# Kernel optimization log

Measured on AMD Instinct MI355X. Metric: run time of the kernel, lower is better.

The kernel has to match this reference:

```python
import jax, jax.numpy as jnp
import numpy as np

DIM = 4096
N_HEADS = 32
N_KV_HEADS = 8
HEAD_DIM = 128
ROPE_THETA = 10000.0
REPEATS = N_HEADS // N_KV_HEADS
SCALE = HEAD_DIM ** -0.5


def rope(x, seq_len, offset):
    # x: [b, h, seq_len, head_dim]; faithful to source: cos/sin from cat((freqs,freqs)),
    # rotate built by interleaved pair swap then flatten.
    d = x.shape[-1]
    inv_freq = 1.0 / (ROPE_THETA ** (jnp.arange(0, d, 2, dtype=jnp.float32) / d))  # [d/2]
    t = jnp.arange(offset, offset + seq_len, dtype=jnp.float32)                    # [L]
    freqs = t[:, None] * inv_freq[None, :]                                         # [L, d/2]
    emb = jnp.concatenate([freqs, freqs], axis=-1)                                 # [L, d]
    cos_emb = jnp.cos(emb)
    sin_emb = jnp.sin(emb)
    x_even = x[..., 0::2]
    x_odd = x[..., 1::2]
    rotate_x = jnp.stack([-x_odd, x_even], axis=-1).reshape(x.shape)
    return x * cos_emb + rotate_x * sin_emb


def setup_inputs() -> dict:
    key = jax.random.key(0)
    k1, k2, k3, k4, k5 = jax.random.split(key, 5)
    b, l = 1, 2048
    s = 0.02
    x = jax.random.normal(k1, (b, l, DIM), dtype=jnp.float32)
    wq = jax.random.normal(k2, (DIM, N_HEADS * HEAD_DIM), dtype=jnp.float32) * s
    wk = jax.random.normal(k3, (DIM, N_KV_HEADS * HEAD_DIM), dtype=jnp.float32) * s
    wv = jax.random.normal(k4, (DIM, N_KV_HEADS * HEAD_DIM), dtype=jnp.float32) * s
    wo = jax.random.normal(k5, (N_HEADS * HEAD_DIM, DIM), dtype=jnp.float32) * s
    return {"x": x, "wq": wq, "wk": wk, "wv": wv, "wo": wo, "seq_len": l}


def reference(x, wq, wk, wv, wo, seq_len):
    b, l, _ = x.shape
    q = (x @ wq).reshape(b, l, N_HEADS, HEAD_DIM).transpose(0, 2, 1, 3)       # [b,H,l,d]
    k = (x @ wk).reshape(b, l, N_KV_HEADS, HEAD_DIM).transpose(0, 2, 1, 3)    # [b,Hk,l,d]
    v = (x @ wv).reshape(b, l, N_KV_HEADS, HEAD_DIM).transpose(0, 2, 1, 3)
    # repeat KV heads to match query heads (GQA)
    k = jnp.repeat(k, REPEATS, axis=1)   # [b,H,l,d]
    v = jnp.repeat(v, REPEATS, axis=1)
    offset = 0  # cache is None
    q = rope(q, seq_len, offset)
    k = rope(k, seq_len, offset)
    scores = jnp.einsum('bhid,bhjd->bhij', q * SCALE, k)
    scores = jax.nn.softmax(scores.astype(jnp.float32), axis=-1).astype(scores.dtype)
    out = jnp.einsum('bhij,bhjd->bhid', scores, v)
    out = out.transpose(0, 2, 1, 3).reshape(b, l, N_HEADS * HEAD_DIM)
    return out @ wo, (k, v)
```

## Files before the change

kernel.cpp:

```cpp
#include <hip/hip_runtime.h>
#include <cstdint>
#include <cstddef>

#define DIM 4096
#define SEQ 2048
#define NH 32
#define NKV 8
#define HD 128
#define QKVN 6144

typedef __bf16 bf16_t;
typedef __bf16 bf16x8 __attribute__((ext_vector_type(8)));
typedef __bf16 bf16x4 __attribute__((ext_vector_type(4)));
typedef __bf16 bf16x2 __attribute__((ext_vector_type(2)));
typedef float f32x4 __attribute__((ext_vector_type(4)));
typedef int int4v __attribute__((ext_vector_type(4)));

__device__ __forceinline__ f32x4 mfma16(bf16x8 a, bf16x8 b, f32x4 c) {
  return __builtin_amdgcn_mfma_f32_16x16x32_bf16(a, b, c, 0, 0, 0);
}

__device__ __forceinline__ void async16(const bf16_t* g, bf16_t* l) {
  __builtin_amdgcn_global_load_lds((__attribute__((address_space(1))) void*)g,
                                   (__attribute__((address_space(3))) void*)l,
                                   16, 0, 0);
}

__device__ __forceinline__ int pack2(float a, float b) {
  bf16x2 h = { (bf16_t)a, (bf16_t)b };
  return __builtin_bit_cast(int, h);
}

#define LGKM0() do { asm volatile("s_waitcnt lgkmcnt(0)" ::: "memory"); \
                     __builtin_amdgcn_sched_barrier(0); } while (0)
#define VM0() do { asm volatile("s_waitcnt vmcnt(0)" ::: "memory"); } while (0)

__global__ void cast_x(const float* __restrict__ x, bf16_t* __restrict__ xb) {
  int i = blockIdx.x * 256 + threadIdx.x;
  const float4 v = ((const float4*)x)[i];
  bf16x4 o = { (bf16_t)v.x, (bf16_t)v.y, (bf16_t)v.z, (bf16_t)v.w };
  *(bf16x4*)(xb + (size_t)i * 4) = o;
}

__global__ void tcast(const float* __restrict__ src, bf16_t* __restrict__ dst,
                      int Ncols, int Kdim) {
  __shared__ float tile[32][33];
  int n0 = blockIdx.x * 32, k0 = blockIdx.y * 32;
  int tx = threadIdx.x, ty = threadIdx.y;
#pragma unroll
  for (int r = 0; r < 4; r++)
    tile[ty + 8 * r][tx] = src[(size_t)(k0 + ty + 8 * r) * Ncols + n0 + tx];
  __syncthreads();
#pragma unroll
  for (int r = 0; r < 4; r++)
    dst[(size_t)(n0 + ty + 8 * r) * Kdim + k0 + tx] = (bf16_t)tile[tx][ty + 8 * r];
}

__global__ __launch_bounds__(512) void gemm256(const bf16_t* __restrict__ A,
                                               const bf16_t* __restrict__ Bt,
                                               float* __restrict__ C,
                                               int M, int N, int K) {
  __shared__ bf16_t As[2][16384];
  __shared__ bf16_t Bs[2][16384];
  const int t = threadIdx.x;
  const int lane = t & 63;
  const int l15 = lane & 15, quad = lane >> 4;
  const int w = t >> 6, wm = w >> 2, wn = w & 3;

  const int gx = gridDim.x;
  const int nwg = gx * gridDim.y;
  const int id = blockIdx.y * gx + blockIdx.x;
  const int swz = (id & 7) * (nwg >> 3) + (id >> 3);
  const int bm = (swz / gx) * 256, bn = (swz % gx) * 256;

  const int srow = t >> 3;
  const int scol = ((t & 7) << 3) ^ ((t >> 1) & 16);
  const bf16_t* gA = A + (size_t)(bm + srow) * K + scol;
  const bf16_t* gB = Bt + (size_t)(bn + srow) * K + scol;
  const int ldst = t * 8;

  const int qx = (quad * 8) ^ ((l15 & 4) ? 16 : 0);
  const int aBase = wm * 8192 + l15 * 64 + qx;
  const int bBase = (wn >> 1) * 8192 + ((wn & 1) * 64 + l15) * 64 + qx;

  f32x4 acc[8][4] = {};
  bf16x8 af[4][2], bfr[2][2];

#pragma unroll
  for (int h = 0; h < 2; h++)
#pragma unroll
    for (int i = 0; i < 2; i++) {
      async16(gA + (size_t)(h * 128 + i * 64) * K, &As[0][h * 8192 + i * 4096 + ldst]);
      async16(gB + (size_t)(h * 128 + i * 64) * K, &Bs[0][h * 8192 + i * 4096 + ldst]);
    }
  VM0();
  __builtin_amdgcn_s_barrier();

  const int nkt = K >> 6;
  for (int kt = 0; kt < nkt; ++kt) {
    const int buf = kt & 1;
    const int k1 = (kt + 1) << 6;
    const bool pf = (kt + 1) < nkt;

#pragma unroll
    for (int mi = 0; mi < 4; mi++)
#pragma unroll
      for (int s = 0; s < 2; s++)
        af[mi][s] = *(const bf16x8*)&As[buf][aBase + mi * 1024 + s * 32];
#pragma unroll
    for (int ni = 0; ni < 2; ni++)
#pragma unroll
      for (int s = 0; s < 2; s++)
        bfr[ni][s] = *(const bf16x8*)&Bs[buf][bBase + ni * 1024 + s * 32];
    if (pf) {
#pragma unroll
      for (int h = 0; h < 2; h++)
#pragma unroll
        for (int i = 0; i < 2; i++)
          async16(gA + (size_t)(h * 128 + i * 64) * K + k1,
                  &As[buf ^ 1][h * 8192 + i * 4096 + ldst]);
    }
    __builtin_amdgcn_s_barrier();
    LGKM0();
    __builtin_amdgcn_s_setprio(1);
#pragma unroll
    for (int mi = 0; mi < 4; mi++)
#pragma unroll
      for (int ni = 0; ni < 2; ni++)
#pragma unroll
        for (int s = 0; s < 2; s++)
          acc[mi][ni] = mfma16(af[mi][s], bfr[ni][s], acc[mi][ni]);
    __builtin_amdgcn_s_setprio(0);
    __builtin_amdgcn_s_barrier();

#pragma unroll
    for (int ni = 0; ni < 2; ni++)
#pragma unroll
      for (int s = 0; s < 2; s++)
        bfr[ni][s] = *(const bf16x8*)&Bs[buf][bBase + (ni + 2) * 1024 + s * 32];
    if (pf) {
#pragma unroll
      for (int h = 0; h < 2; h++)
#pragma unroll
        for (int i = 0; i < 2; i++)
          async16(gB + (size_t)(h * 128 + i * 64) * K + k1,
                  &Bs[buf ^ 1][h * 8192 + i * 4096 + ldst]);
    }
    __builtin_amdgcn_s_barrier();
    LGKM0();
    __builtin_amdgcn_s_setprio(1);
#pragma unroll
    for (int mi = 0; mi < 4; mi++)
#pragma unroll
      for (int ni = 0; ni < 2; ni++)
#pragma unroll
        for (int s = 0; s < 2; s++)
          acc[mi][ni + 2] = mfma16(af[mi][s], bfr[ni][s], acc[mi][ni + 2]);
    __builtin_amdgcn_s_setprio(0);
    __builtin_amdgcn_s_barrier();

#pragma unroll
    for (int mi = 0; mi < 4; mi++)
#pragma unroll
      for (int s = 0; s < 2; s++)
        af[mi][s] = *(const bf16x8*)&As[buf][aBase + (mi + 4) * 1024 + s * 32];
    __builtin_amdgcn_s_barrier();
    LGKM0();
    __builtin_amdgcn_s_setprio(1);
#pragma unroll
    for (int mi = 0; mi < 4; mi++)
#pragma unroll
      for (int ni = 0; ni < 2; ni++)
#pragma unroll
        for (int s = 0; s < 2; s++)
          acc[mi + 4][ni + 2] = mfma16(af[mi][s], bfr[ni][s], acc[mi + 4][ni + 2]);
    __builtin_amdgcn_s_setprio(0);
    __builtin_amdgcn_s_barrier();

#pragma unroll
    for (int ni = 0; ni < 2; ni++)
#pragma unroll
      for (int s = 0; s < 2; s++)
        bfr[ni][s] = *(const bf16x8*)&Bs[buf][bBase + ni * 1024 + s * 32];
    __builtin_amdgcn_s_barrier();
    LGKM0();
    __builtin_amdgcn_s_setprio(1);
#pragma unroll
    for (int mi = 0; mi < 4; mi++)
#pragma unroll
      for (int ni = 0; ni < 2; ni++)
#pragma unroll
        for (int s = 0; s < 2; s++)
          acc[mi + 4][ni] = mfma16(af[mi][s], bfr[ni][s], acc[mi + 4][ni]);
    __builtin_amdgcn_s_setprio(0);
    VM0();
    __builtin_amdgcn_s_barrier();
  }

#pragma unroll
  for (int mi = 0; mi < 8; mi++)
#pragma unroll
    for (int ni = 0; ni < 4; ni++) {
      size_t row = (size_t)bm + wm * 128 + mi * 16 + quad * 4;
      size_t col = (size_t)bn + wn * 64 + ni * 16 + l15;
#pragma unroll
      for (int r = 0; r < 4; r++)
        C[(row + r) * N + col] = acc[mi][ni][r];
    }
}

__global__ void rope_scatter(const float* __restrict__ qkv, bf16_t* __restrict__ Qb,
                             bf16_t* __restrict__ Kb, bf16_t* __restrict__ Vt,
                             float* __restrict__ kOut, float* __restrict__ vOut) {
  int idx = blockIdx.x * 256 + threadIdx.x;
  int t = idx / 3072;
  int p = idx - t * 3072;
  const float NEG_L2T_64 = -0.20762050593046f;
  const float SS = 0.08838834764831845f * 1.4426950408889634f;
  if (p < 2048) {
    int hh = p >> 6, pr = p & 63;
    int d0 = pr << 1;
    const float* src = qkv + (size_t)t * QKVN + hh * HD + d0;
    float a = src[0], b = src[1];
    int j0 = d0 & 63, j1 = (d0 + 1) & 63;
    float th0 = (float)t * exp2f((float)j0 * NEG_L2T_64);
    float th1 = (float)t * exp2f((float)j1 * NEG_L2T_64);
    float o0 = (a * cosf(th0) - b * sinf(th0)) * SS;
    float o1 = (b * cosf(th1) + a * sinf(th1)) * SS;
    bf16_t* dst = Qb + ((size_t)hh * SEQ + t) * HD + d0;
    dst[0] = (bf16_t)o0;
    dst[1] = (bf16_t)o1;
  } else if (p < 2560) {
    int q2 = p - 2048;
    int kh = q2 >> 6, pr = q2 & 63;
    int d0 = pr << 1;
    const float* src = qkv + (size_t)t * QKVN + 4096 + kh * HD + d0;
    float a = src[0], b = src[1];
    int j0 = d0 & 63, j1 = (d0 + 1) & 63;
    float th0 = (float)t * exp2f((float)j0 * NEG_L2T_64);
    float th1 = (float)t * exp2f((float)j1 * NEG_L2T_64);
    float o0 = a * cosf(th0) - b * sinf(th0);
    float o1 = b * cosf(th1) + a * sinf(th1);
    bf16_t* dst = Kb + ((size_t)kh * SEQ + t) * HD + d0;
    dst[0] = (bf16_t)o0;
    dst[1] = (bf16_t)o1;
#pragma unroll
    for (int rep = 0; rep < 4; rep++) {
      float* kp = kOut + ((size_t)(kh * 4 + rep) * SEQ + t) * HD + d0;
      kp[0] = o0;
      kp[1] = o1;
    }
  } else {
    int q2 = p - 2560;
    int kh = q2 >> 6, pr = q2 & 63;
    int d0 = pr << 1;
    const float* src = qkv + (size_t)t * QKVN + 5120 + kh * HD + d0;
    float a = src[0], b = src[1];
#pragma unroll
    for (int rep = 0; rep < 4; rep++) {
      float* vp = vOut + ((size_t)(kh * 4 + rep) * SEQ + t) * HD + d0;
      vp[0] = a;
      vp[1] = b;
    }
    int tp = (t & ~31) + ((t & 12) << 1) + (t & 3) + ((t & 16) >> 2);
    Vt[((size_t)kh * HD + d0) * SEQ + tp] = (bf16_t)a;
    Vt[((size_t)kh * HD + d0 + 1) * SEQ + tp] = (bf16_t)b;
  }
}

__global__ __launch_bounds__(512, 2) void attn_kernel(const bf16_t* __restrict__ Qb,
                                                      const bf16_t* __restrict__ Kb,
                                                      const bf16_t* __restrict__ Vt,
                                                      bf16_t* __restrict__ AO) {
  __shared__ bf16_t Ks[2][8192];
  __shared__ bf16_t Vs[2][8192];
  const int h = blockIdx.y, kh = h >> 2;
  const int qbase = blockIdx.x * 256;
  const int w = threadIdx.x >> 6, lane = threadIdx.x & 63;
  const int l15 = lane & 15, quad = lane >> 4;
  const bf16_t* KbH = Kb + (size_t)kh * SEQ * HD;
  const bf16_t* VtH = Vt + (size_t)kh * HD * SEQ;

  bf16x8 qf[2][4];
#pragma unroll
  for (int nq = 0; nq < 2; nq++) {
    const bf16_t* qp = Qb + ((size_t)h * SEQ + qbase + w * 32 + nq * 16 + l15) * HD + quad * 8;
#pragma unroll
    for (int kc = 0; kc < 4; kc++) qf[nq][kc] = *(const bf16x8*)(qp + kc * 32);
  }

  f32x4 acc[8][2] = {};
  float rsum[2] = {0.f, 0.f};

  auto stage = [&](int buf, int kt0) {
    if (w < 4) {
      int kc = w;
#pragma unroll
      for (int kg = 0; kg < 4; kg++) {
        const bf16_t* g = KbH + (size_t)(kt0 + kg * 16 + (lane >> 2)) * HD + kc * 32 + (lane & 3) * 8;
        async16(g, &Ks[buf][kc * 2048 + kg * 512]);
      }
    } else {
      int vi = w - 4, kt = vi >> 1, dg0 = (vi & 1) * 4;
#pragma unroll
      for (int j = 0; j < 4; j++) {
        int dg = dg0 + j;
        const bf16_t* g = VtH + (size_t)(dg * 16 + (lane >> 2)) * SEQ + kt0 + kt * 32 + (lane & 3) * 8;
        async16(g, &Vs[buf][kt * 4096 + dg * 512]);
      }
    }
  };

  stage(0, 0);
  int buf = 0;

  for (int kt0 = 0; kt0 < SEQ; kt0 += 64, buf ^= 1) {
    __syncthreads();
    if (kt0 + 64 < SEQ) stage(buf ^ 1, kt0 + 64);

    f32x4 sacc[4][2] = {};
#pragma unroll
    for (int mi = 0; mi < 4; mi++)
#pragma unroll
      for (int kc = 0; kc < 4; kc++) {
        bf16x8 kf = *(const bf16x8*)(&Ks[buf][(kc * 64 + mi * 16 + l15) * 32 + quad * 8]);
#pragma unroll
        for (int nq = 0; nq < 2; nq++)
          sacc[mi][nq] = mfma16(kf, qf[nq][kc], sacc[mi][nq]);
      }

    int pk[4][2][2];
#pragma unroll
    for (int mi = 0; mi < 4; mi++)
#pragma unroll
      for (int nq = 0; nq < 2; nq++) {
        float p0 = exp2f(sacc[mi][nq][0]);
        float p1 = exp2f(sacc[mi][nq][1]);
        float p2 = exp2f(sacc[mi][nq][2]);
        float p3 = exp2f(sacc[mi][nq][3]);
        rsum[nq] += (p0 + p1) + (p2 + p3);
        pk[mi][nq][0] = pack2(p0, p1);
        pk[mi][nq][1] = pack2(p2, p3);
      }

#pragma unroll
    for (int kt = 0; kt < 2; kt++) {
#pragma unroll
      for (int nq = 0; nq < 2; nq++) {
        int4v dw;
        dw[0] = pk[2 * kt][nq][0];
        dw[1] = pk[2 * kt][nq][1];
        dw[2] = pk[2 * kt + 1][nq][0];
        dw[3] = pk[2 * kt + 1][nq][1];
        bf16x8 pf = __builtin_bit_cast(bf16x8, dw);
#pragma unroll
        for (int dt = 0; dt < 8; dt++) {
          bf16x8 vf = *(const bf16x8*)(&Vs[buf][(kt * 128 + dt * 16 + l15) * 32 + quad * 8]);
          acc[dt][nq] = mfma16(vf, pf, acc[dt][nq]);
        }
      }
    }
  }

#pragma unroll
  for (int nq = 0; nq < 2; nq++) {
    float rs = rsum[nq];
    rs += __shfl_xor(rs, 16);
    rs += __shfl_xor(rs, 32);
    float inv = 1.0f / rs;
    int q = qbase + w * 32 + nq * 16 + l15;
#pragma unroll
    for (int dt = 0; dt < 8; dt++) {
      bf16x4 o = { (bf16_t)(acc[dt][nq][0] * inv), (bf16_t)(acc[dt][nq][1] * inv),
                   (bf16_t)(acc[dt][nq][2] * inv), (bf16_t)(acc[dt][nq][3] * inv) };
      *(bf16x4*)(AO + (size_t)q * DIM + h * HD + dt * 16 + quad * 4) = o;
    }
  }
}

extern "C" void kernel_launch(void* const* d_in, const int* in_sizes, int n_in,
                              void* d_out, int out_size, void* d_ws, size_t ws_size,
                              hipStream_t stream) {
  const float* x = (const float*)d_in[0];
  const float* wq = (const float*)d_in[1];
  const float* wk = (const float*)d_in[2];
  const float* wv = (const float*)d_in[3];
  const float* wo = (const float*)d_in[4];
  float* out = (float*)d_out;
  float* kOut = out + (size_t)SEQ * DIM;
  float* vOut = kOut + (size_t)NH * SEQ * HD;

  char* ws = (char*)d_ws;
  bf16_t* Xb = (bf16_t*)ws;
  bf16_t* WT = (bf16_t*)(ws + 16777216);
  float* QKV = (float*)(ws + 67108864);
  bf16_t* WoT = (bf16_t*)(ws + 67108864);
  bf16_t* Qb = (bf16_t*)(ws + 117440512);
  bf16_t* Kb = (bf16_t*)(ws + 134217728);
  bf16_t* Vt = (bf16_t*)(ws + 138412032);
  bf16_t* AO = Xb;

  dim3 tb(32, 8);
  cast_x<<<8192, 256, 0, stream>>>(x, Xb);
  tcast<<<dim3(128, 128), tb, 0, stream>>>(wq, WT, 4096, 4096);
  tcast<<<dim3(32, 128), tb, 0, stream>>>(wk, WT + (size_t)4096 * 4096, 1024, 4096);
  tcast<<<dim3(32, 128), tb, 0, stream>>>(wv, WT + (size_t)5120 * 4096, 1024, 4096);
  gemm256<<<dim3(24, 8), 512, 0, stream>>>(Xb, WT, QKV, 2048, 6144, 4096);
  rope_scatter<<<24576, 256, 0, stream>>>(QKV, Qb, Kb, Vt, kOut, vOut);
  tcast<<<dim3(128, 128), tb, 0, stream>>>(wo, WoT, 4096, 4096);
  attn_kernel<<<dim3(8, 32), 512, 0, stream>>>(Qb, Kb, Vt, AO);
  gemm256<<<dim3(16, 8), 512, 0, stream>>>(AO, WoT, out, 2048, 4096, 4096);
}
```

Before: 607.5 us.

## Shrink GEMM N-tile to 192/128 columns and stage loads with partial vmcnt waits

The bf16 GEMM is templated on the N-tile width, so the QKV projection uses 256x192 tiles and the output projection uses 256x128 tiles. Both grids grow to 256 workgroups, which fills more compute units than the earlier 192 and 128 tiles. The LDS swizzle becomes a row-based XOR, and the per-stage prefetches are split into three groups with partial vmcnt waits in place of a full drain. The cost is more total global traffic from the narrower tiles, and the hand-counted waits are fragile.

```diff
diff --git a/kernel.cpp b/kernel.cpp
--- a/kernel.cpp
+++ b/kernel.cpp
@@ -33,7 +33,14 @@
 
 #define LGKM0() do { asm volatile("s_waitcnt lgkmcnt(0)" ::: "memory"); \
                      __builtin_amdgcn_sched_barrier(0); } while (0)
-#define VM0() do { asm volatile("s_waitcnt vmcnt(0)" ::: "memory"); } while (0)
+
+template <int N> __device__ __forceinline__ void vmw() {
+  if constexpr (N == 3) asm volatile("s_waitcnt vmcnt(3)" ::: "memory");
+  else if constexpr (N == 4) asm volatile("s_waitcnt vmcnt(4)" ::: "memory");
+  else if constexpr (N == 5) asm volatile("s_waitcnt vmcnt(5)" ::: "memory");
+  else if constexpr (N == 6) asm volatile("s_waitcnt vmcnt(6)" ::: "memory");
+  __builtin_amdgcn_sched_barrier(0);
+}
 
 __global__ void cast_x(const float* __restrict__ x, bf16_t* __restrict__ xb) {
   int i = blockIdx.x * 256 + threadIdx.x;
@@ -56,44 +63,54 @@
     dst[(size_t)(n0 + ty + 8 * r) * Kdim + k0 + tx] = (bf16_t)tile[tx][ty + 8 * r];
 }
 
+template <int NF>
 __global__ __launch_bounds__(512) void gemm256(const bf16_t* __restrict__ A,
                                                const bf16_t* __restrict__ Bt,
                                                float* __restrict__ C,
                                                int M, int N, int K) {
+  constexpr int NA = NF - 1;
+  constexpr int S1 = 2 + NA;
   __shared__ bf16_t As[2][16384];
-  __shared__ bf16_t Bs[2][16384];
+  __shared__ bf16_t Bs[2][NF * 4096];
   const int t = threadIdx.x;
   const int lane = t & 63;
   const int l15 = lane & 15, quad = lane >> 4;
   const int w = t >> 6, wm = w >> 2, wn = w & 3;
+  const int cgx = l15 & 7;
 
   const int gx = gridDim.x;
   const int nwg = gx * gridDim.y;
   const int id = blockIdx.y * gx + blockIdx.x;
   const int swz = (id & 7) * (nwg >> 3) + (id >> 3);
-  const int bm = (swz / gx) * 256, bn = (swz % gx) * 256;
+  const int bm = (swz / gx) * 256, bn = (swz % gx) * (NF * 64);
 
   const int srow = t >> 3;
-  const int scol = ((t & 7) << 3) ^ ((t >> 1) & 16);
+  const int scol = ((t & 7) ^ (srow & 7)) << 3;
   const bf16_t* gA = A + (size_t)(bm + srow) * K + scol;
   const bf16_t* gB = Bt + (size_t)(bn + srow) * K + scol;
   const int ldst = t * 8;
 
-  const int qx = (quad * 8) ^ ((l15 & 4) ? 16 : 0);
-  const int aBase = wm * 8192 + l15 * 64 + qx;
-  const int bBase = (wn >> 1) * 8192 + ((wn & 1) * 64 + l15) * 64 + qx;
-
-  f32x4 acc[8][4] = {};
-  bf16x8 af[4][2], bfr[2][2];
-
-#pragma unroll
-  for (int h = 0; h < 2; h++)
-#pragma unroll
-    for (int i = 0; i < 2; i++) {
-      async16(gA + (size_t)(h * 128 + i * 64) * K, &As[0][h * 8192 + i * 4096 + ldst]);
-      async16(gB + (size_t)(h * 128 + i * 64) * K, &Bs[0][h * 8192 + i * 4096 + ldst]);
-    }
-  VM0();
+  f32x4 acc[8][NF] = {};
+  bf16x8 af[4][2], bfa[NA][2], bfb[2];
+
+  auto sb1 = [&](int b2, int kk) {
+    async16(gA + kk, &As[b2][ldst]);
+    async16(gA + (size_t)64 * K + kk, &As[b2][4096 + ldst]);
+    async16(gB + kk, &Bs[b2][ldst]);
+    if constexpr (NF == 3) async16(gB + (size_t)64 * K + kk, &Bs[b2][4096 + ldst]);
+  };
+  auto sb2 = [&](int b2, int kk) {
+    async16(gB + (size_t)((NF - 1) * 64) * K + kk, &Bs[b2][(NF - 1) * 4096 + ldst]);
+  };
+  auto sb3 = [&](int b2, int kk) {
+    async16(gA + (size_t)128 * K + kk, &As[b2][8192 + ldst]);
+    async16(gA + (size_t)192 * K + kk, &As[b2][12288 + ldst]);
+  };
+
+  sb1(0, 0);
+  sb2(0, 0);
+  sb3(0, 0);
+  vmw<3>();
   __builtin_amdgcn_s_barrier();
 
   const int nkt = K >> 6;
@@ -106,103 +123,91 @@
     for (int mi = 0; mi < 4; mi++)
 #pragma unroll
       for (int s = 0; s < 2; s++)
-        af[mi][s] = *(const bf16x8*)&As[buf][aBase + mi * 1024 + s * 32];
-#pragma unroll
-    for (int ni = 0; ni < 2; ni++)
-#pragma unroll
-      for (int s = 0; s < 2; s++)
-        bfr[ni][s] = *(const bf16x8*)&Bs[buf][bBase + ni * 1024 + s * 32];
-    if (pf) {
-#pragma unroll
-      for (int h = 0; h < 2; h++)
-#pragma unroll
-        for (int i = 0; i < 2; i++)
-          async16(gA + (size_t)(h * 128 + i * 64) * K + k1,
-                  &As[buf ^ 1][h * 8192 + i * 4096 + ldst]);
-    }
+        af[mi][s] = *(const bf16x8*)&As[buf][(wm * 64 + mi * 16 + l15) * 64 +
+                                            (((s << 2) | quad) ^ cgx) * 8];
+#pragma unroll
+    for (int ni = 0; ni < NA; ni++)
+#pragma unroll
+      for (int s = 0; s < 2; s++)
+        bfa[ni][s] = *(const bf16x8*)&Bs[buf][(ni * 64 + wn * 16 + l15) * 64 +
+                                              (((s << 2) | quad) ^ cgx) * 8];
+    if (pf) sb1(buf ^ 1, k1);
     __builtin_amdgcn_s_barrier();
     LGKM0();
     __builtin_amdgcn_s_setprio(1);
 #pragma unroll
     for (int mi = 0; mi < 4; mi++)
 #pragma unroll
-      for (int ni = 0; ni < 2; ni++)
+      for (int ni = 0; ni < NA; ni++)
 #pragma unroll
         for (int s = 0; s < 2; s++)
-          acc[mi][ni] = mfma16(af[mi][s], bfr[ni][s], acc[mi][ni]);
+          acc[mi][ni] = mfma16(af[mi][s], bfa[ni][s], acc[mi][ni]);
     __builtin_amdgcn_s_setprio(0);
-    __builtin_amdgcn_s_barrier();
-
-#pragma unroll
-    for (int ni = 0; ni < 2; ni++)
-#pragma unroll
-      for (int s = 0; s < 2; s++)
-        bfr[ni][s] = *(const bf16x8*)&Bs[buf][bBase + (ni + 2) * 1024 + s * 32];
-    if (pf) {
-#pragma unroll
-      for (int h = 0; h < 2; h++)
-#pragma unroll
-        for (int i = 0; i < 2; i++)
-          async16(gB + (size_t)(h * 128 + i * 64) * K + k1,
-                  &Bs[buf ^ 1][h * 8192 + i * 4096 + ldst]);
-    }
+    vmw<2 + S1>();
+    __builtin_amdgcn_s_barrier();
+
+#pragma unroll
+    for (int s = 0; s < 2; s++)
+      bfb[s] = *(const bf16x8*)&Bs[buf][((NF - 1) * 64 + wn * 16 + l15) * 64 +
+                                        (((s << 2) | quad) ^ cgx) * 8];
+    if (pf) sb2(buf ^ 1, k1);
     __builtin_amdgcn_s_barrier();
     LGKM0();
     __builtin_amdgcn_s_setprio(1);
 #pragma unroll
     for (int mi = 0; mi < 4; mi++)
 #pragma unroll
-      for (int ni = 0; ni < 2; ni++)
-#pragma unroll
-        for (int s = 0; s < 2; s++)
-          acc[mi][ni + 2] = mfma16(af[mi][s], bfr[ni][s], acc[mi][ni + 2]);
+      for (int s = 0; s < 2; s++)
+        acc[mi][NF - 1] = mfma16(af[mi][s], bfb[s], acc[mi][NF - 1]);
     __builtin_amdgcn_s_setprio(0);
-    __builtin_amdgcn_s_barrier();
-
-#pragma unroll
-    for (int mi = 0; mi < 4; mi++)
-#pragma unroll
-      for (int s = 0; s < 2; s++)
-        af[mi][s] = *(const bf16x8*)&As[buf][aBase + (mi + 4) * 1024 + s * 32];
+    vmw<1 + S1>();
+    __builtin_amdgcn_s_barrier();
+
+#pragma unroll
+    for (int mi = 0; mi < 4; mi++)
+#pragma unroll
+      for (int s = 0; s < 2; s++)
+        af[mi][s] = *(const bf16x8*)&As[buf][(128 + wm * 64 + mi * 16 + l15) * 64 +
+                                             (((s << 2) | quad) ^ cgx) * 8];
+    if (pf) sb3(buf ^ 1, k1);
     __builtin_amdgcn_s_barrier();
     LGKM0();
     __builtin_amdgcn_s_setprio(1);
 #pragma unroll
     for (int mi = 0; mi < 4; mi++)
 #pragma unroll
-      for (int ni = 0; ni < 2; ni++)
-#pragma unroll
-        for (int s = 0; s < 2; s++)
-          acc[mi + 4][ni + 2] = mfma16(af[mi][s], bfr[ni][s], acc[mi + 4][ni + 2]);
+      for (int s = 0; s < 2; s++)
+        acc[mi + 4][NF - 1] = mfma16(af[mi][s], bfb[s], acc[mi + 4][NF - 1]);
     __builtin_amdgcn_s_setprio(0);
     __builtin_amdgcn_s_barrier();
 
 #pragma unroll
-    for (int ni = 0; ni < 2; ni++)
-#pragma unroll
-      for (int s = 0; s < 2; s++)
-        bfr[ni][s] = *(const bf16x8*)&Bs[buf][bBase + ni * 1024 + s * 32];
+    for (int ni = 0; ni < NA; ni++)
+#pragma unroll
+      for (int s = 0; s < 2; s++)
+        bfa[ni][s] = *(const bf16x8*)&Bs[buf][(ni * 64 + wn * 16 + l15) * 64 +
+                                              (((s << 2) | quad) ^ cgx) * 8];
     __builtin_amdgcn_s_barrier();
     LGKM0();
     __builtin_amdgcn_s_setprio(1);
 #pragma unroll
     for (int mi = 0; mi < 4; mi++)
 #pragma unroll
-      for (int ni = 0; ni < 2; ni++)
+      for (int ni = 0; ni < NA; ni++)
 #pragma unroll
         for (int s = 0; s < 2; s++)
-          acc[mi + 4][ni] = mfma16(af[mi][s], bfr[ni][s], acc[mi + 4][ni]);
+          acc[mi + 4][ni] = mfma16(af[mi][s], bfa[ni][s], acc[mi + 4][ni]);
     __builtin_amdgcn_s_setprio(0);
-    VM0();
+    vmw<3>();
     __builtin_amdgcn_s_barrier();
   }
 
 #pragma unroll
   for (int mi = 0; mi < 8; mi++)
 #pragma unroll
-    for (int ni = 0; ni < 4; ni++) {
-      size_t row = (size_t)bm + wm * 128 + mi * 16 + quad * 4;
-      size_t col = (size_t)bn + wn * 64 + ni * 16 + l15;
+    for (int ni = 0; ni < NF; ni++) {
+      size_t row = (size_t)bm + (mi >> 2) * 128 + wm * 64 + (mi & 3) * 16 + quad * 4;
+      size_t col = (size_t)bn + ni * 64 + wn * 16 + l15;
 #pragma unroll
       for (int r = 0; r < 4; r++)
         C[(row + r) * N + col] = acc[mi][ni][r];
@@ -405,9 +410,9 @@
   tcast<<<dim3(128, 128), tb, 0, stream>>>(wq, WT, 4096, 4096);
   tcast<<<dim3(32, 128), tb, 0, stream>>>(wk, WT + (size_t)4096 * 4096, 1024, 4096);
   tcast<<<dim3(32, 128), tb, 0, stream>>>(wv, WT + (size_t)5120 * 4096, 1024, 4096);
-  gemm256<<<dim3(24, 8), 512, 0, stream>>>(Xb, WT, QKV, 2048, 6144, 4096);
+  gemm256<3><<<dim3(32, 8), 512, 0, stream>>>(Xb, WT, QKV, 2048, 6144, 4096);
   rope_scatter<<<24576, 256, 0, stream>>>(QKV, Qb, Kb, Vt, kOut, vOut);
   tcast<<<dim3(128, 128), tb, 0, stream>>>(wo, WoT, 4096, 4096);
   attn_kernel<<<dim3(8, 32), 512, 0, stream>>>(Qb, Kb, Vt, AO);
-  gemm256<<<dim3(16, 8), 512, 0, stream>>>(AO, WoT, out, 2048, 4096, 4096);
-}
+  gemm256<2><<<dim3(32, 8), 512, 0, stream>>>(AO, WoT, out, 2048, 4096, 4096);
+}
```

New measurement: 552.1 us. 9.1% less time.

## Split output GEMM along K and pipeline per-half-K stage loads with finer waits

Applied to the files above, without the earlier changes.

The 256x256 GEMM now stages each 64-wide K tile as two 32-wide halves with a new XOR swizzle. It prefetches the next tile half by half and waits with vmcnt(4) instead of draining all loads, so copies overlap the MFMA phases more. The output projection GEMM gains split-K over two z-slices, raising its grid from 128 to 256 workgroups. A separate add kernel then reduces the partial sum. This trades an extra 32 MB partial write/read and one more launch for better CU occupancy on a 256-CU device.

```diff
diff --git a/kernel.cpp b/kernel.cpp
--- a/kernel.cpp
+++ b/kernel.cpp
@@ -33,7 +33,8 @@
 
 #define LGKM0() do { asm volatile("s_waitcnt lgkmcnt(0)" ::: "memory"); \
                      __builtin_amdgcn_sched_barrier(0); } while (0)
-#define VM0() do { asm volatile("s_waitcnt vmcnt(0)" ::: "memory"); } while (0)
+#define VMW4() do { asm volatile("s_waitcnt vmcnt(4)" ::: "memory"); \
+                    __builtin_amdgcn_sched_barrier(0); } while (0)
 
 __global__ void cast_x(const float* __restrict__ x, bf16_t* __restrict__ xb) {
   int i = blockIdx.x * 256 + threadIdx.x;
@@ -59,7 +60,8 @@
 __global__ __launch_bounds__(512) void gemm256(const bf16_t* __restrict__ A,
                                                const bf16_t* __restrict__ Bt,
                                                float* __restrict__ C,
-                                               int M, int N, int K) {
+                                               float* __restrict__ Cp,
+                                               int M, int N, int K, int Kloc) {
   __shared__ bf16_t As[2][16384];
   __shared__ bf16_t Bs[2][16384];
   const int t = threadIdx.x;
@@ -72,141 +74,123 @@
   const int id = blockIdx.y * gx + blockIdx.x;
   const int swz = (id & 7) * (nwg >> 3) + (id >> 3);
   const int bm = (swz / gx) * 256, bn = (swz % gx) * 256;
-
-  const int srow = t >> 3;
-  const int scol = ((t & 7) << 3) ^ ((t >> 1) & 16);
-  const bf16_t* gA = A + (size_t)(bm + srow) * K + scol;
-  const bf16_t* gB = Bt + (size_t)(bn + srow) * K + scol;
+  const int kbase = blockIdx.z * Kloc;
+  float* __restrict__ Cd = blockIdx.z ? Cp : C;
+
+  const int srow = t >> 2;
+  const int gcol = ((t & 3) ^ (srow & 3)) << 3;
+  const bf16_t* gA = A + (size_t)(bm + srow) * K + kbase + gcol;
+  const bf16_t* gB = Bt + (size_t)(bn + srow) * K + kbase + gcol;
   const int ldst = t * 8;
 
-  const int qx = (quad * 8) ^ ((l15 & 4) ? 16 : 0);
-  const int aBase = wm * 8192 + l15 * 64 + qx;
-  const int bBase = (wn >> 1) * 8192 + ((wn & 1) * 64 + l15) * 64 + qx;
+  const int fcol = ((quad ^ (l15 & 3)) << 3);
 
   f32x4 acc[8][4] = {};
-  bf16x8 af[4][2], bfr[2][2];
-
-#pragma unroll
-  for (int h = 0; h < 2; h++)
-#pragma unroll
-    for (int i = 0; i < 2; i++) {
-      async16(gA + (size_t)(h * 128 + i * 64) * K, &As[0][h * 8192 + i * 4096 + ldst]);
-      async16(gB + (size_t)(h * 128 + i * 64) * K, &Bs[0][h * 8192 + i * 4096 + ldst]);
-    }
-  VM0();
+  bf16x8 af[4], bfr[4][2];
+
+  auto stKh = [&](int b2, int s, int kk) {
+    async16(gA + kk + s * 32, &As[b2][s * 8192 + ldst]);
+    async16(gA + (size_t)128 * K + kk + s * 32, &As[b2][s * 8192 + 4096 + ldst]);
+    async16(gB + kk + s * 32, &Bs[b2][s * 8192 + ldst]);
+    async16(gB + (size_t)128 * K + kk + s * 32, &Bs[b2][s * 8192 + 4096 + ldst]);
+  };
+
+  stKh(0, 0, 0);
+  stKh(0, 1, 0);
+  VMW4();
   __builtin_amdgcn_s_barrier();
 
-  const int nkt = K >> 6;
+  const int nkt = Kloc >> 6;
   for (int kt = 0; kt < nkt; ++kt) {
-    const int buf = kt & 1;
-    const int k1 = (kt + 1) << 6;
-    const bool pf = (kt + 1) < nkt;
-
-#pragma unroll
-    for (int mi = 0; mi < 4; mi++)
-#pragma unroll
-      for (int s = 0; s < 2; s++)
-        af[mi][s] = *(const bf16x8*)&As[buf][aBase + mi * 1024 + s * 32];
-#pragma unroll
-    for (int ni = 0; ni < 2; ni++)
-#pragma unroll
-      for (int s = 0; s < 2; s++)
-        bfr[ni][s] = *(const bf16x8*)&Bs[buf][bBase + ni * 1024 + s * 32];
-    if (pf) {
-#pragma unroll
-      for (int h = 0; h < 2; h++)
-#pragma unroll
-        for (int i = 0; i < 2; i++)
-          async16(gA + (size_t)(h * 128 + i * 64) * K + k1,
-                  &As[buf ^ 1][h * 8192 + i * 4096 + ldst]);
-    }
+    const int b2 = kt & 1, bn2 = b2 ^ 1;
+    const int kn = (kt + 1 == nkt) ? 0 : (kt + 1) << 6;
+
+#pragma unroll
+    for (int mi = 0; mi < 4; mi++)
+      af[mi] = *(const bf16x8*)&As[b2][(wm * 128 + mi * 16 + l15) * 32 + fcol];
+#pragma unroll
+    for (int ni = 0; ni < 4; ni++)
+      bfr[ni][0] = *(const bf16x8*)&Bs[b2][(wn * 64 + ni * 16 + l15) * 32 + fcol];
+    stKh(bn2, 0, kn);
     __builtin_amdgcn_s_barrier();
     LGKM0();
     __builtin_amdgcn_s_setprio(1);
 #pragma unroll
     for (int mi = 0; mi < 4; mi++)
 #pragma unroll
-      for (int ni = 0; ni < 2; ni++)
-#pragma unroll
-        for (int s = 0; s < 2; s++)
-          acc[mi][ni] = mfma16(af[mi][s], bfr[ni][s], acc[mi][ni]);
+      for (int ni = 0; ni < 4; ni++)
+        acc[mi][ni] = mfma16(af[mi], bfr[ni][0], acc[mi][ni]);
     __builtin_amdgcn_s_setprio(0);
-    __builtin_amdgcn_s_barrier();
-
-#pragma unroll
-    for (int ni = 0; ni < 2; ni++)
-#pragma unroll
-      for (int s = 0; s < 2; s++)
-        bfr[ni][s] = *(const bf16x8*)&Bs[buf][bBase + (ni + 2) * 1024 + s * 32];
-    if (pf) {
-#pragma unroll
-      for (int h = 0; h < 2; h++)
-#pragma unroll
-        for (int i = 0; i < 2; i++)
-          async16(gB + (size_t)(h * 128 + i * 64) * K + k1,
-                  &Bs[buf ^ 1][h * 8192 + i * 4096 + ldst]);
-    }
+    VMW4();
+    __builtin_amdgcn_s_barrier();
+
+#pragma unroll
+    for (int mi = 0; mi < 4; mi++)
+      af[mi] = *(const bf16x8*)&As[b2][8192 + (wm * 128 + mi * 16 + l15) * 32 + fcol];
+#pragma unroll
+    for (int ni = 0; ni < 4; ni++)
+      bfr[ni][1] = *(const bf16x8*)&Bs[b2][8192 + (wn * 64 + ni * 16 + l15) * 32 + fcol];
+    stKh(bn2, 1, kn);
     __builtin_amdgcn_s_barrier();
     LGKM0();
     __builtin_amdgcn_s_setprio(1);
 #pragma unroll
     for (int mi = 0; mi < 4; mi++)
 #pragma unroll
-      for (int ni = 0; ni < 2; ni++)
-#pragma unroll
-        for (int s = 0; s < 2; s++)
-          acc[mi][ni + 2] = mfma16(af[mi][s], bfr[ni][s], acc[mi][ni + 2]);
+      for (int ni = 0; ni < 4; ni++)
+        acc[mi][ni] = mfma16(af[mi], bfr[ni][1], acc[mi][ni]);
     __builtin_amdgcn_s_setprio(0);
     __builtin_amdgcn_s_barrier();
 
 #pragma unroll
     for (int mi = 0; mi < 4; mi++)
-#pragma unroll
-      for (int s = 0; s < 2; s++)
-        af[mi][s] = *(const bf16x8*)&As[buf][aBase + (mi + 4) * 1024 + s * 32];
+      af[mi] = *(const bf16x8*)&As[b2][(wm * 128 + 64 + mi * 16 + l15) * 32 + fcol];
     __builtin_amdgcn_s_barrier();
     LGKM0();
     __builtin_amdgcn_s_setprio(1);
 #pragma unroll
     for (int mi = 0; mi < 4; mi++)
 #pragma unroll
-      for (int ni = 0; ni < 2; ni++)
-#pragma unroll
-        for (int s = 0; s < 2; s++)
-          acc[mi + 4][ni + 2] = mfma16(af[mi][s], bfr[ni][s], acc[mi + 4][ni + 2]);
+      for (int ni = 0; ni < 4; ni++)
+        acc[mi + 4][ni] = mfma16(af[mi], bfr[ni][0], acc[mi + 4][ni]);
     __builtin_amdgcn_s_setprio(0);
     __builtin_amdgcn_s_barrier();
 
 #pragma unroll
-    for (int ni = 0; ni < 2; ni++)
-#pragma unroll
-      for (int s = 0; s < 2; s++)
-        bfr[ni][s] = *(const bf16x8*)&Bs[buf][bBase + ni * 1024 + s * 32];
+    for (int mi = 0; mi < 4; mi++)
+      af[mi] = *(const bf16x8*)&As[b2][8192 + (wm * 128 + 64 + mi * 16 + l15) * 32 + fcol];
     __builtin_amdgcn_s_barrier();
     LGKM0();
     __builtin_amdgcn_s_setprio(1);
 #pragma unroll
     for (int mi = 0; mi < 4; mi++)
 #pragma unroll
-      for (int ni = 0; ni < 2; ni++)
-#pragma unroll
-        for (int s = 0; s < 2; s++)
-          acc[mi + 4][ni] = mfma16(af[mi][s], bfr[ni][s], acc[mi + 4][ni]);
+      for (int ni = 0; ni < 4; ni++)
+        acc[mi + 4][ni] = mfma16(af[mi], bfr[ni][1], acc[mi + 4][ni]);
     __builtin_amdgcn_s_setprio(0);
-    VM0();
-    __builtin_amdgcn_s_barrier();
-  }
-
-#pragma unroll
-  for (int mi = 0; mi < 8; mi++)
+    VMW4();
+    __builtin_amdgcn_s_barrier();
+  }
+
+#pragma unroll
+  for (int m8 = 0; m8 < 8; m8++)
 #pragma unroll
     for (int ni = 0; ni < 4; ni++) {
-      size_t row = (size_t)bm + wm * 128 + mi * 16 + quad * 4;
+      size_t row = (size_t)bm + wm * 128 + (m8 >> 2) * 64 + (m8 & 3) * 16 + quad * 4;
       size_t col = (size_t)bn + wn * 64 + ni * 16 + l15;
 #pragma unroll
       for (int r = 0; r < 4; r++)
-        C[(row + r) * N + col] = acc[mi][ni][r];
-    }
+        Cd[(row + r) * N + col] = acc[m8][ni][r];
+    }
+  asm volatile("s_waitcnt vmcnt(0)" ::: "memory");
+}
+
+__global__ void addf4(float* __restrict__ o, const float* __restrict__ p) {
+  int i = blockIdx.x * 256 + threadIdx.x;
+  float4 a = ((const float4*)o)[i];
+  const float4 b = ((const float4*)p)[i];
+  a.x += b.x; a.y += b.y; a.z += b.z; a.w += b.w;
+  ((float4*)o)[i] = a;
 }
 
 __global__ void rope_scatter(const float* __restrict__ qkv, bf16_t* __restrict__ Qb,
@@ -393,6 +377,7 @@
   char* ws = (char*)d_ws;
   bf16_t* Xb = (bf16_t*)ws;
   bf16_t* WT = (bf16_t*)(ws + 16777216);
+  float* Cp1 = (float*)(ws + 16777216);
   float* QKV = (float*)(ws + 67108864);
   bf16_t* WoT = (bf16_t*)(ws + 67108864);
   bf16_t* Qb = (bf16_t*)(ws + 117440512);
@@ -405,9 +390,10 @@
   tcast<<<dim3(128, 128), tb, 0, stream>>>(wq, WT, 4096, 4096);
   tcast<<<dim3(32, 128), tb, 0, stream>>>(wk, WT + (size_t)4096 * 4096, 1024, 4096);
   tcast<<<dim3(32, 128), tb, 0, stream>>>(wv, WT + (size_t)5120 * 4096, 1024, 4096);
-  gemm256<<<dim3(24, 8), 512, 0, stream>>>(Xb, WT, QKV, 2048, 6144, 4096);
+  gemm256<<<dim3(24, 8, 1), 512, 0, stream>>>(Xb, WT, QKV, nullptr, 2048, 6144, 4096, 4096);
   rope_scatter<<<24576, 256, 0, stream>>>(QKV, Qb, Kb, Vt, kOut, vOut);
   tcast<<<dim3(128, 128), tb, 0, stream>>>(wo, WoT, 4096, 4096);
   attn_kernel<<<dim3(8, 32), 512, 0, stream>>>(Qb, Kb, Vt, AO);
-  gemm256<<<dim3(16, 8), 512, 0, stream>>>(AO, WoT, out, 2048, 4096, 4096);
-}
+  gemm256<<<dim3(16, 8, 2), 512, 0, stream>>>(AO, WoT, out, Cp1, 2048, 4096, 4096, 2048);
+  addf4<<<8192, 256, 0, stream>>>(out, Cp1);
+}
```

Result: faster. 578.8 us (-4.7%).
